# Optimization experiments

Measured on AMD Instinct MI355X. Metric: run time of the kernel, lower is better.

The kernel has to match this reference:

```python
import jax, jax.numpy as jnp
import numpy as np

SIGMA = 0.05
SIGMA2 = SIGMA * SIGMA
N_NODES = 100000
N_EDGES = 3200000


def setup_inputs() -> dict:
    key = jax.random.key(0)
    k1, k2, k3, k4 = jax.random.split(key, 4)
    source_points = jax.random.normal(k1, (N_NODES, 3), dtype=jnp.float32)
    target_points = jax.random.normal(k2, (N_NODES, 3), dtype=jnp.float32)
    edge_index = jax.random.randint(k3, (2, N_EDGES), 0, N_NODES, dtype=jnp.int64)
    edge_weights = jax.random.uniform(k4, (N_EDGES, 1), dtype=jnp.float32)
    return {"source_points": source_points, "target_points": target_points,
            "edge_index": edge_index, "edge_weights": edge_weights}


def reference(source_points, target_points, edge_index, edge_weights):
    N = source_points.shape[0]
    dst = edge_index[0]  # center point each edge contributes to
    nbr = edge_index[1]  # neighbor point index

    src_nb = source_points[nbr]            # [E,3]
    tgt_nb = target_points[nbr]            # [E,3]

    ones_e = jnp.ones((edge_index.shape[1],), dtype=source_points.dtype)
    counts = jnp.maximum(jax.ops.segment_sum(ones_e, dst, num_segments=N), 1.0)[:, None]
    src_centers = jax.ops.segment_sum(src_nb, dst, num_segments=N) / counts  # [N,3]
    tgt_centers = jax.ops.segment_sum(tgt_nb, dst, num_segments=N) / counts  # [N,3]

    src_diff = (src_nb - src_centers[dst]) * edge_weights  # [E,3]
    tgt_diff = tgt_nb - tgt_centers[dst]                   # [E,3]

    # per-edge outer product, scattered to per-point 3x3 covariances
    edge_mats = src_diff[:, :, None] * tgt_diff[:, None, :]          # [E,3,3]
    point_mats = jax.ops.segment_sum(edge_mats, dst, num_segments=N)  # [N,3,3]

    U, S, Vh = jnp.linalg.svd(point_mats)  # torch.svd's V = Vh^T, so U @ V^T == U @ Vh
    R0 = jnp.matmul(U, Vh)
    det = jnp.linalg.det(R0)
    ones_n = jnp.ones((N,), dtype=source_points.dtype)
    d_diag = jax.lax.stop_gradient(jnp.stack([ones_n, ones_n, det], axis=-1))  # [N,3]
    R = jnp.matmul(U * d_diag[:, None, :], Vh)  # U @ diag(d) @ Vh, proper rotation

    trans = tgt_centers - jnp.einsum('nij,nj->ni', R, src_centers)  # [N,3]

    # apply each neighbor's rigid transform and compute robust weights
    transformed = jnp.einsum('eij,ej->ei', R[nbr], src_nb) + trans[nbr]  # [E,3]
    d2 = jnp.sum(jnp.square(transformed - tgt_nb), axis=-1, keepdims=True)  # [E,1]
    new_edge_weights = SIGMA2 / (d2 + SIGMA2)
    return (R, trans, new_edge_weights)
```

## Files before the change

### kernel.cpp

```cpp
#include <hip/hip_runtime.h>
#include <math.h>

static constexpr float kSigma2 = 0.05f * 0.05f;
static constexpr int kCap2 = 2560;

__device__ __forceinline__ int load_idx(const void* ei, long long j, int is64) {
    if (is64) return (int)(((const long long*)ei)[j]);
    return ((const int*)ei)[j];
}

__global__ void k_detect(const int* __restrict__ ei32, int E, int* __restrict__ nz) {
    int t = threadIdx.x;
    int lim = E < 2048 ? E : 2048;
    int acc = 0;
    for (int k = t; k < lim; k += blockDim.x) acc |= ei32[2 * k + 1];
    if (acc) atomicOr(nz, 1);
}

__global__ void k_pack(const float* __restrict__ src, const float* __restrict__ tgt,
                       float4* __restrict__ s4, float4* __restrict__ t4, int N) {
    int i = blockIdx.x * blockDim.x + threadIdx.x;
    if (i >= N) return;
    s4[i] = make_float4(src[3 * i + 0], src[3 * i + 1], src[3 * i + 2], 0.0f);
    t4[i] = make_float4(tgt[3 * i + 0], tgt[3 * i + 1], tgt[3 * i + 2], 0.0f);
}

__device__ void kabsch_from_M(const double M[3][3], double Rm[3][3]) {
    Rm[0][0] = 1; Rm[0][1] = 0; Rm[0][2] = 0;
    Rm[1][0] = 0; Rm[1][1] = 1; Rm[1][2] = 0;
    Rm[2][0] = 0; Rm[2][1] = 0; Rm[2][2] = 1;

    double frob2 = 0.0;
#pragma unroll
    for (int r = 0; r < 3; ++r)
#pragma unroll
        for (int c = 0; c < 3; ++c) frob2 += M[r][c] * M[r][c];
    if (frob2 <= 1e-80) return;

    double A[3][3];
#pragma unroll
    for (int r = 0; r < 3; ++r)
#pragma unroll
        for (int c = 0; c < 3; ++c) {
            double s = 0.0;
#pragma unroll
            for (int k = 0; k < 3; ++k) s += M[k][r] * M[k][c];
            A[r][c] = s;
        }
    double V[3][3] = {{1, 0, 0}, {0, 1, 0}, {0, 0, 1}};
    const int PL[3] = {0, 0, 1};
    const int QL[3] = {1, 2, 2};
    for (int sweep = 0; sweep < 15; ++sweep) {
        double off = fabs(A[0][1]) + fabs(A[0][2]) + fabs(A[1][2]);
        if (off == 0.0) break;
        for (int pi = 0; pi < 3; ++pi) {
            int p = PL[pi], q = QL[pi], r3 = 3 - p - q;
            double apq = A[p][q];
            if (apq == 0.0) continue;
            double theta = (A[q][q] - A[p][p]) / (2.0 * apq);
            double t = copysign(1.0, theta) / (fabs(theta) + sqrt(theta * theta + 1.0));
            double c = 1.0 / sqrt(t * t + 1.0);
            double s = t * c;
            A[p][p] -= t * apq;
            A[q][q] += t * apq;
            A[p][q] = 0.0; A[q][p] = 0.0;
            double arp = A[r3][p], arq = A[r3][q];
            A[r3][p] = c * arp - s * arq; A[p][r3] = A[r3][p];
            A[r3][q] = s * arp + c * arq; A[q][r3] = A[r3][q];
#pragma unroll
            for (int k = 0; k < 3; ++k) {
                double vp = V[k][p], vq = V[k][q];
                V[k][p] = c * vp - s * vq;
                V[k][q] = s * vp + c * vq;
            }
        }
    }
    double lam[3] = {A[0][0], A[1][1], A[2][2]};
    int id0 = 0, id1 = 1, id2 = 2, tt;
    if (lam[id0] < lam[id1]) { tt = id0; id0 = id1; id1 = tt; }
    if (lam[id0] < lam[id2]) { tt = id0; id0 = id2; id2 = tt; }
    if (lam[id1] < lam[id2]) { tt = id1; id1 = id2; id2 = tt; }
    double v1[3] = {V[0][id0], V[1][id0], V[2][id0]};
    double v2[3] = {V[0][id1], V[1][id1], V[2][id1]};
    double v3[3] = {V[0][id2], V[1][id2], V[2][id2]};

    double b1[3], b2[3];
#pragma unroll
    for (int r = 0; r < 3; ++r) {
        b1[r] = M[r][0] * v1[0] + M[r][1] * v1[1] + M[r][2] * v1[2];
        b2[r] = M[r][0] * v2[0] + M[r][1] * v2[1] + M[r][2] * v2[2];
    }
    double n1 = sqrt(b1[0] * b1[0] + b1[1] * b1[1] + b1[2] * b1[2]);
    if (n1 <= 1e-150) return;
    double u1[3] = {b1[0] / n1, b1[1] / n1, b1[2] / n1};
    double dot = u1[0] * b2[0] + u1[1] * b2[1] + u1[2] * b2[2];
    double w2[3] = {b2[0] - dot * u1[0], b2[1] - dot * u1[1], b2[2] - dot * u1[2]};
    double n2 = sqrt(w2[0] * w2[0] + w2[1] * w2[1] + w2[2] * w2[2]);
    double u2[3];
    if (n2 > n1 * 1e-12) {
        u2[0] = w2[0] / n2; u2[1] = w2[1] / n2; u2[2] = w2[2] / n2;
    } else {
        double ex0 = (fabs(u1[0]) < 0.9) ? 1.0 : 0.0;
        double ex1 = 1.0 - ex0;
        double cx = u1[1] * 0.0 - u1[2] * ex1;
        double cy = u1[2] * ex0 - u1[0] * 0.0;
        double cz = u1[0] * ex1 - u1[1] * ex0;
        double cn = sqrt(cx * cx + cy * cy + cz * cz);
        u2[0] = cx / cn; u2[1] = cy / cn; u2[2] = cz / cn;
    }
    double u3[3] = {u1[1] * u2[2] - u1[2] * u2[1],
                    u1[2] * u2[0] - u1[0] * u2[2],
                    u1[0] * u2[1] - u1[1] * u2[0]};
    double dV = v1[0] * (v2[1] * v3[2] - v2[2] * v3[1])
              - v1[1] * (v2[0] * v3[2] - v2[2] * v3[0])
              + v1[2] * (v2[0] * v3[1] - v2[1] * v3[0]);
    dV = (dV >= 0.0) ? 1.0 : -1.0;
#pragma unroll
    for (int r = 0; r < 3; ++r)
#pragma unroll
        for (int c = 0; c < 3; ++c)
            Rm[r][c] = u1[r] * v1[c] + u2[r] * v2[c] + dV * u3[r] * v3[c];
}


__global__ void __launch_bounds__(256) k_bhist(const void* __restrict__ ei,
                                               int* __restrict__ thist,
                                               int* __restrict__ ccnt,
                                               const int* __restrict__ nz,
                                               int E, int N, int nbuckets,
                                               int ntiles16, int ntiles4) {
    __shared__ int lhist[2048];
    __shared__ int ccl[4][16];
    int t = threadIdx.x;
    int lane = t & 63;
    long long tile = (long long)blockIdx.x * 16384;
    long long remll = (long long)E - tile;
    int rem = (remll < 16384) ? (int)remll : 16384;
    int is64 = (*nz == 0);
    for (int i = t; i < 2048; i += 256) lhist[i] = 0;
    if (t < 64) ((int*)ccl)[t] = 0;
    __syncthreads();
    if (rem == 16384) {
        for (int it = 0; it < 8; ++it) {
            long long base = tile + (long long)it * 2048 + (long long)t * 8;
            int d[8];
            if (is64) {
                const long long* p = (const long long*)ei + base;
#pragma unroll
                for (int k = 0; k < 4; ++k) {
                    longlong2 v = ((const longlong2*)p)[k];
                    d[2 * k] = (int)v.x;
                    d[2 * k + 1] = (int)v.y;
                }
            } else {
                const int* p = (const int*)ei + base;
                int4 a = ((const int4*)p)[0];
                int4 bb = ((const int4*)p)[1];
                d[0] = a.x; d[1] = a.y; d[2] = a.z; d[3] = a.w;
                d[4] = bb.x; d[5] = bb.y; d[6] = bb.z; d[7] = bb.w;
            }
            int sub = it >> 1;
#pragma unroll
            for (int k = 0; k < 8; ++k) {
                int dk = d[k];
                int bin = ((unsigned)dk < (unsigned)N) ? (dk >> 13) : -1;
                if (bin >= 0) atomicAdd(&lhist[dk >> 6], 1);
                unsigned long long valid = __ballot(bin >= 0);
                unsigned long long v0 = __ballot(bin & 1);
                unsigned long long v1 = __ballot(bin & 2);
                unsigned long long v2 = __ballot(bin & 4);
                unsigned long long v3 = __ballot(bin & 8);
                if (lane < 16) {
                    unsigned long long m = valid;
                    m &= (lane & 1) ? v0 : ~v0;
                    m &= (lane & 2) ? v1 : ~v1;
                    m &= (lane & 4) ? v2 : ~v2;
                    m &= (lane & 8) ? v3 : ~v3;
                    int c = __popcll(m);
                    if (c > 0) atomicAdd(&ccl[sub][lane], c);
                }
            }
        }
    } else {
        for (int idx = t; idx < rem; idx += 256) {
            int dk = load_idx(ei, tile + idx, is64);
            if ((unsigned)dk < (unsigned)N) {
                atomicAdd(&lhist[dk >> 6], 1);
                atomicAdd(&ccl[idx >> 12][dk >> 13], 1);
            }
        }
    }
    __syncthreads();
    int* row = thist + (long long)blockIdx.x * 2048;
    for (int b = t; b < 2048; b += 256) row[b] = lhist[b];
    if (t < 64) {
        int sub = t >> 4, c = t & 15;
        long long st = (long long)blockIdx.x * 4 + sub;
        if (st < ntiles4) ccnt[st * 16 + c] = ccl[sub][c];
    }
}

__global__ void __launch_bounds__(256) k_bsum(const int* __restrict__ thist,
                                              int* __restrict__ btot, int ntiles16) {
    int t = threadIdx.x;
    int bin = blockIdx.x * 16 + (t >> 4);
    int j = t & 15;
    int s = 0;
    for (int i = j; i < ntiles16; i += 16) s += thist[(long long)i * 2048 + bin];
#pragma unroll
    for (int off = 8; off >= 1; off >>= 1) s += __shfl_down(s, off, 16);
    if (j == 0) btot[bin] = s;
}

__global__ void k_scan(const int* __restrict__ btot, int* __restrict__ boff,
                       int* __restrict__ cur16, int* __restrict__ curC16, int nbuckets) {
    __shared__ int sm[2048];
    int t = threadIdx.x;
    int v0 = (t < nbuckets) ? btot[t] : 0;
    int v1 = (t + 1024 < nbuckets) ? btot[t + 1024] : 0;
    sm[t] = v0;
    sm[t + 1024] = v1;
    __syncthreads();
    for (int s = 1; s < 2048; s <<= 1) {
        int x0 = (t >= s) ? sm[t - s] : 0;
        int x1 = (t + 1024 >= s) ? sm[t + 1024 - s] : 0;
        __syncthreads();
        sm[t] += x0;
        sm[t + 1024] += x1;
        __syncthreads();
    }
    if (t < nbuckets) {
        int ex = sm[t] - v0;
        boff[t] = ex;
        cur16[t * 16] = ex;
        if ((t & 127) == 0) curC16[(t >> 7) * 16] = ex;
    }
    int t2 = t + 1024;
    if (t2 < nbuckets) {
        int ex = sm[t2] - v1;
        boff[t2] = ex;
        cur16[t2 * 16] = ex;
        if ((t2 & 127) == 0) curC16[(t2 >> 7) * 16] = ex;
    }
    if (t == nbuckets - 1) boff[nbuckets] = sm[t];
    if (t2 == nbuckets - 1) boff[nbuckets] = sm[t2];
}

__global__ void __launch_bounds__(256) k_cscan(const int* __restrict__ ccnt,
                                               const int* __restrict__ boff,
                                               int* __restrict__ cbase,
                                               int ntiles, int nbuckets, int ncoarse) {
    __shared__ int sm[256];
    int c = blockIdx.x;
    int t = threadIdx.x;
    int f = c * 128;
    if (f > nbuckets) f = nbuckets;
    int run = boff[f];
    for (int start = 0; start < ntiles; start += 256) {
        int i = start + t;
        int v = (i < ntiles) ? ccnt[(long long)i * 16 + c] : 0;
        sm[t] = v;
        __syncthreads();
        for (int s = 1; s < 256; s <<= 1) {
            int x = (t >= s) ? sm[t - s] : 0;
            __syncthreads();
            sm[t] += x;
            __syncthreads();
        }
        if (i < ntiles) cbase[(long long)i * 16 + c] = run + sm[t] - v;
        int tot = sm[255];
        __syncthreads();
        run += tot;
    }
}

__global__ void __launch_bounds__(256) k_cscatter(const void* __restrict__ ei,
                                                  const float* __restrict__ ew,
                                                  const int* __restrict__ cbase,
                                                  int2* __restrict__ sedge1,
                                                  const int* __restrict__ nz,
                                                  int E, int N, int ncoarse) {
    __shared__ int2 stage[4096];
    __shared__ unsigned char binOf[4096];
    __shared__ int hist[16];
    __shared__ int excl[16];
    __shared__ int gbase[16];
    __shared__ int woffs[4][16];
    __shared__ int wbase[4][16];
    int t = threadIdx.x;
    int w = t >> 6, lane = t & 63;
    unsigned long long lanebelow = ((unsigned long long)1 << lane) - 1;
    long long tile = (long long)blockIdx.x * 4096;
    long long remll = (long long)E - tile;
    int rem = (remll < 4096) ? (int)remll : 4096;
    int is64 = (*nz == 0);
    if (t < 16) hist[t] = 0;
    if (t < 64) ((int*)woffs)[t] = 0;
    __syncthreads();

    int mybin[16];
    int mypos[16];
    int2 mypay[16];
#pragma unroll
    for (int h = 0; h < 2; ++h) {
        int dd[8], nn[8];
        float ww[8];
        int cnt8 = 0;
        int coff = h * 2048 + t * 8;
        long long cb = tile + coff;
        if (coff + 8 <= rem) {
            if (is64) {
                const long long* pd = (const long long*)ei + cb;
                const long long* pn = (const long long*)ei + (long long)E + cb;
#pragma unroll
                for (int k = 0; k < 4; ++k) {
                    longlong2 vd = ((const longlong2*)pd)[k];
                    longlong2 vn = ((const longlong2*)pn)[k];
                    dd[2 * k] = (int)vd.x; dd[2 * k + 1] = (int)vd.y;
                    nn[2 * k] = (int)vn.x; nn[2 * k + 1] = (int)vn.y;
                }
            } else {
                const int* pd = (const int*)ei + cb;
                const int* pn = (const int*)ei + (long long)E + cb;
                int4 a = ((const int4*)pd)[0], b = ((const int4*)pd)[1];
                int4 c = ((const int4*)pn)[0], d = ((const int4*)pn)[1];
                dd[0] = a.x; dd[1] = a.y; dd[2] = a.z; dd[3] = a.w;
                dd[4] = b.x; dd[5] = b.y; dd[6] = b.z; dd[7] = b.w;
                nn[0] = c.x; nn[1] = c.y; nn[2] = c.z; nn[3] = c.w;
                nn[4] = d.x; nn[5] = d.y; nn[6] = d.z; nn[7] = d.w;
            }
            const float* pw = ew + cb;
            float4 wa = ((const float4*)pw)[0], wb = ((const float4*)pw)[1];
            ww[0] = wa.x; ww[1] = wa.y; ww[2] = wa.z; ww[3] = wa.w;
            ww[4] = wb.x; ww[5] = wb.y; ww[6] = wb.z; ww[7] = wb.w;
            cnt8 = 8;
        } else {
#pragma unroll
            for (int k = 0; k < 8; ++k) {
                if (coff + k < rem) {
                    dd[cnt8] = load_idx(ei, cb + k, is64);
                    nn[cnt8] = load_idx(ei, (long long)E + cb + k, is64);
                    ww[cnt8] = ew[cb + k];
                    ++cnt8;
                }
            }
        }
#pragma unroll
        for (int k = 0; k < 8; ++k) {
            int r = h * 8 + k;
            int bin = -1;
            if (k < cnt8) {
                int d = dd[k];
                if ((unsigned)d < (unsigned)N) {
                    int n = nn[k];
                    if ((unsigned)n >= (unsigned)N) n = N;
                    bin = d >> 13;
                    mypay[r].x = (n << 13) | (d & 8191);
                    mypay[r].y = __float_as_int(ww[k]);
                }
            }
            mybin[r] = bin;
            unsigned long long valid = __ballot(bin >= 0);
            unsigned long long v0 = __ballot(bin & 1);
            unsigned long long v1 = __ballot(bin & 2);
            unsigned long long v2 = __ballot(bin & 4);
            unsigned long long v3 = __ballot(bin & 8);
            if (bin >= 0) {
                unsigned long long m = valid;
                m &= (bin & 1) ? v0 : ~v0;
                m &= (bin & 2) ? v1 : ~v1;
                m &= (bin & 4) ? v2 : ~v2;
                m &= (bin & 8) ? v3 : ~v3;
                int rank = __popcll(m & lanebelow);
                int cnt = __popcll(m);
                int cur = woffs[w][bin];
                mypos[r] = cur + rank;
                if (rank == 0) woffs[w][bin] = cur + cnt;
            }
        }
    }
    __syncthreads();
    if (t < 64) {
        int w2 = t >> 4, b = t & 15;
        int c = woffs[w2][b];
        wbase[w2][b] = (c > 0) ? atomicAdd(&hist[b], c) : 0;
    }
    __syncthreads();
    if (t == 0) {
        int run = 0;
#pragma unroll
        for (int c = 0; c < 16; ++c) { excl[c] = run; run += hist[c]; }
    }
    __syncthreads();
#pragma unroll
    for (int r = 0; r < 16; ++r) {
        if (mybin[r] >= 0) {
            int lpos = excl[mybin[r]] + wbase[w][mybin[r]] + mypos[r];
            stage[lpos] = mypay[r];
            binOf[lpos] = (unsigned char)mybin[r];
        }
    }
    if (t < 16) gbase[t] = cbase[(long long)blockIdx.x * 16 + t];
    __syncthreads();
    int total = excl[15] + hist[15];
    for (int lpos = t; lpos < total; lpos += 256) {
        int c = binOf[lpos];
        sedge1[(long long)gbase[c] + (lpos - excl[c])] = stage[lpos];
    }
}

__global__ void __launch_bounds__(256) k_fscatter(const int2* __restrict__ sedge1,
                                                  int* __restrict__ cur16,
                                                  const int* __restrict__ boff,
                                                  int2* __restrict__ sedge2,
                                                  int E, int nbuckets, int ncoarse) {
    __shared__ int2 stage[2048];
    __shared__ unsigned short binOf[2048];
    __shared__ int lhist[1024];
    __shared__ int lincl[1024];
    __shared__ int gbase[1024];
    __shared__ int co[17];
    __shared__ int s_clo, s_W;
    int t = threadIdx.x;
    if (t <= ncoarse) {
        int f = t * 128;
        if (f > nbuckets) f = nbuckets;
        co[t] = boff[f];
    }
    __syncthreads();
    int Ev = co[ncoarse];
    long long tile = (long long)blockIdx.x * 2048;
    if (tile >= Ev) return;
    long long remll = (long long)Ev - tile;
    int rem = (remll < 2048) ? (int)remll : 2048;

    if (t == 0) {
        long long p0 = tile, p1 = tile + rem - 1;
        int c0 = 0;
        while (c0 + 1 < ncoarse && p0 >= co[c0 + 1]) ++c0;
        int c1 = c0;
        while (c1 + 1 < ncoarse && p1 >= co[c1 + 1]) ++c1;
        s_clo = c0;
        s_W = (c1 - c0 + 1) * 128;
    }
    __syncthreads();
    int clo = s_clo, W = s_W;

    int2 pay[8];
    int cnt8 = 0;
    if (rem == 2048) {
        const int4* p4 = (const int4*)(sedge1 + tile + (long long)t * 8);
#pragma unroll
        for (int k = 0; k < 4; ++k) {
            int4 v = p4[k];
            pay[2 * k].x = v.x; pay[2 * k].y = v.y;
            pay[2 * k + 1].x = v.z; pay[2 * k + 1].y = v.w;
        }
        cnt8 = 8;
    } else {
        int base = t * 8;
#pragma unroll
        for (int k = 0; k < 8; ++k) {
            int idx = base + k;
            if (idx < rem) pay[cnt8++] = sedge1[tile + idx];
        }
    }

    if (W > 1024) {
        for (int k = 0; k < cnt8; ++k) {
            long long pos = tile + t * 8 + k;
            int c = clo;
            while (c + 1 < ncoarse && pos >= co[c + 1]) ++c;
            int x1 = pay[k].x;
            unsigned nbr = ((unsigned)x1) >> 13;
            int fin = c * 128 + ((x1 & 8191) >> 6);
            int gpos = atomicAdd(&cur16[fin * 16], 1);
            int2 out;
            out.x = (int)((nbr << 6) | (unsigned)(x1 & 63));
            out.y = pay[k].y;
            sedge2[gpos] = out;
        }
        return;
    }

    for (int i = t; i < W; i += 256) lhist[i] = 0;
    __syncthreads();

    int mybin[8], myrank[8];
    int2 mypay[8];
#pragma unroll
    for (int k = 0; k < 8; ++k) {
        mybin[k] = -1;
        if (k < cnt8) {
            long long pos = tile + t * 8 + k;
            int c = clo;
            while (c + 1 < ncoarse && pos >= co[c + 1]) ++c;
            int x1 = pay[k].x;
            unsigned nbr = ((unsigned)x1) >> 13;
            int rel = (c - clo) * 128 + ((x1 & 8191) >> 6);
            mybin[k] = rel;
            myrank[k] = atomicAdd(&lhist[rel], 1);
            mypay[k].x = (int)((nbr << 6) | (unsigned)(x1 & 63));
            mypay[k].y = pay[k].y;
        }
    }
    __syncthreads();
    for (int i = t; i < W; i += 256) lincl[i] = lhist[i];
    __syncthreads();
    for (int s = 1; s < W; s <<= 1) {
        int tmp[4];
        int cj = 0;
        for (int i = t; i < W; i += 256) tmp[cj++] = (i >= s) ? lincl[i - s] : 0;
        __syncthreads();
        cj = 0;
        for (int i = t; i < W; i += 256) lincl[i] += tmp[cj++];
        __syncthreads();
    }
#pragma unroll
    for (int k = 0; k < 8; ++k) {
        if (mybin[k] >= 0) {
            int ex = lincl[mybin[k]] - lhist[mybin[k]];
            int lpos = ex + myrank[k];
            stage[lpos] = mypay[k];
            binOf[lpos] = (unsigned short)mybin[k];
        }
    }
    __syncthreads();
    for (int rel = t; rel < W; rel += 256) {
        int c = lhist[rel];
        int fin = clo * 128 + rel;
        gbase[rel] = (c > 0 && fin < nbuckets) ? atomicAdd(&cur16[fin * 16], c) : 0;
    }
    __syncthreads();
    int total = lincl[W - 1];
    for (int lpos = t; lpos < total; lpos += 256) {
        int rel = binOf[lpos];
        int ex = lincl[rel] - lhist[rel];
        sedge2[gbase[rel] + (lpos - ex)] = stage[lpos];
    }
}

__global__ void __launch_bounds__(256) k_binscatter(const void* __restrict__ ei,
                                                    const float* __restrict__ ew,
                                                    int* __restrict__ cur16,
                                                    int2* __restrict__ sedge,
                                                    const int* __restrict__ nz,
                                                    int E, int N, int nbuckets) {
    __shared__ int2 stage[2048];
    __shared__ unsigned short binOf[2048];
    __shared__ int lhist[2048];
    __shared__ int lincl[2048];
    __shared__ int gbase[2048];
    int t = threadIdx.x;
    long long tile = (long long)blockIdx.x * 2048;
    long long remll = (long long)E - tile;
    int rem = (remll < 2048) ? (int)remll : 2048;
    int is64 = (*nz == 0);
    for (int i = t; i < 2048; i += 256) lhist[i] = 0;
    __syncthreads();

    int dd[8], nn[8];
    float ww[8];
    int cnt8 = 0;
    if (rem == 2048) {
        if (is64) {
            const long long* pd = (const long long*)ei + tile + (long long)t * 8;
            const long long* pn = (const long long*)ei + (long long)E + tile + (long long)t * 8;
#pragma unroll
            for (int k = 0; k < 4; ++k) {
                longlong2 vd = ((const longlong2*)pd)[k];
                longlong2 vn = ((const longlong2*)pn)[k];
                dd[2 * k] = (int)vd.x; dd[2 * k + 1] = (int)vd.y;
                nn[2 * k] = (int)vn.x; nn[2 * k + 1] = (int)vn.y;
            }
        } else {
            const int* pd = (const int*)ei + tile + (long long)t * 8;
            const int* pn = (const int*)ei + (long long)E + tile + (long long)t * 8;
            int4 a = ((const int4*)pd)[0], b = ((const int4*)pd)[1];
            int4 c = ((const int4*)pn)[0], d = ((const int4*)pn)[1];
            dd[0] = a.x; dd[1] = a.y; dd[2] = a.z; dd[3] = a.w;
            dd[4] = b.x; dd[5] = b.y; dd[6] = b.z; dd[7] = b.w;
            nn[0] = c.x; nn[1] = c.y; nn[2] = c.z; nn[3] = c.w;
            nn[4] = d.x; nn[5] = d.y; nn[6] = d.z; nn[7] = d.w;
        }
        const float* pw = ew + tile + (long long)t * 8;
        float4 wa = ((const float4*)pw)[0], wb = ((const float4*)pw)[1];
        ww[0] = wa.x; ww[1] = wa.y; ww[2] = wa.z; ww[3] = wa.w;
        ww[4] = wb.x; ww[5] = wb.y; ww[6] = wb.z; ww[7] = wb.w;
        cnt8 = 8;
    } else {
        int base = t * 8;
#pragma unroll
        for (int k = 0; k < 8; ++k) {
            int idx = base + k;
            if (idx < rem) {
                long long e = tile + idx;
                dd[cnt8] = load_idx(ei, e, is64);
                nn[cnt8] = load_idx(ei, (long long)E + e, is64);
                ww[cnt8] = ew[e];
                ++cnt8;
            }
        }
    }

    int mybin[8];
    int myrank[8];
    int2 mypay[8];
#pragma unroll
    for (int k = 0; k < 8; ++k) {
        mybin[k] = -1;
        if (k < cnt8) {
            int d = dd[k];
            if ((unsigned)d < (unsigned)N) {
                int n = nn[k];
                if ((unsigned)n >= (unsigned)N) n = N;
                int bb = d >> 6;
                mybin[k] = bb;
                myrank[k] = atomicAdd(&lhist[bb], 1);
                mypay[k].x = (n << 6) | (d & 63);
                mypay[k].y = __float_as_int(ww[k]);
            }
        }
    }
    __syncthreads();
    for (int i = t; i < 2048; i += 256) lincl[i] = lhist[i];
    __syncthreads();
    for (int s = 1; s < 2048; s <<= 1) {
        int tmp[8];
#pragma unroll
        for (int j = 0; j < 8; ++j) {
            int i = (j << 8) + t;
            tmp[j] = (i >= s) ? lincl[i - s] : 0;
        }
        __syncthreads();
#pragma unroll
        for (int j = 0; j < 8; ++j) {
            int i = (j << 8) + t;
            lincl[i] += tmp[j];
        }
        __syncthreads();
    }
#pragma unroll
    for (int k = 0; k < 8; ++k) {
        if (mybin[k] >= 0) {
            int ex = lincl[mybin[k]] - lhist[mybin[k]];
            int lpos = ex + myrank[k];
            stage[lpos] = mypay[k];
            binOf[lpos] = (unsigned short)mybin[k];
        }
    }
    __syncthreads();
    for (int bb = t; bb < 2048; bb += 256) {
        int c = lhist[bb];
        gbase[bb] = (c > 0 && bb < nbuckets) ? atomicAdd(&cur16[bb * 16], c) : 0;
    }
    __syncthreads();
    int total = lincl[2047];
    for (int lpos = t; lpos < total; lpos += 256) {
        int bb = binOf[lpos];
        int ex = lincl[bb] - lhist[bb];
        sedge[gbase[bb] + (lpos - ex)] = stage[lpos];
    }
}

__global__ void __launch_bounds__(256) k_sortmoment(const int* __restrict__ boff,
                                                    const int2* __restrict__ sedge2,
                                                    const float4* __restrict__ s4,
                                                    const float4* __restrict__ t4,
                                                    float* __restrict__ momG, int N) {
    __shared__ int2 sorted[kCap2];
    __shared__ int hist[64];
    __shared__ int offs[64];
    __shared__ int scanbuf[64];
    __shared__ int woffs[4][64];
    __shared__ int wbase[4][64];
    int b = blockIdx.x, t = threadIdx.x;
    int w = t >> 6, lane = t & 63;
    unsigned long long lanebelow = ((unsigned long long)1 << lane) - 1;
    int e0 = boff[b], e1 = boff[b + 1];
    int cnt = e1 - e0;
    int inlds = (cnt <= kCap2);
    if (t < 64) hist[t] = 0;
    ((int*)woffs)[t] = 0;
    __syncthreads();
    if (inlds) {
        int2 pay[10];
        int mypos[10];
#pragma unroll
        for (int r = 0; r < 10; ++r) {
            int idx = r * 256 + t;
            int bin = -1;
            if (idx < cnt) {
                pay[r] = sedge2[e0 + idx];
                bin = pay[r].x & 63;
            }
            unsigned long long vm = __ballot(bin >= 0);
            unsigned long long b0 = __ballot(bin & 1);
            unsigned long long b1 = __ballot(bin & 2);
            unsigned long long b2 = __ballot(bin & 4);
            unsigned long long b3 = __ballot(bin & 8);
            unsigned long long b4 = __ballot(bin & 16);
            unsigned long long b5 = __ballot(bin & 32);
            if (bin >= 0) {
                unsigned long long m = vm;
                m &= (bin & 1) ? b0 : ~b0;
                m &= (bin & 2) ? b1 : ~b1;
                m &= (bin & 4) ? b2 : ~b2;
                m &= (bin & 8) ? b3 : ~b3;
                m &= (bin & 16) ? b4 : ~b4;
                m &= (bin & 32) ? b5 : ~b5;
                int rank = __popcll(m & lanebelow);
                int cm = __popcll(m);
                int curv = woffs[w][bin];
                mypos[r] = curv + rank;
                if (rank == 0) woffs[w][bin] = curv + cm;
            }
        }
        __syncthreads();
        {
            int w2 = t >> 6, bb = t & 63;
            int c = woffs[w2][bb];
            wbase[w2][bb] = (c > 0) ? atomicAdd(&hist[bb], c) : 0;
        }
        __syncthreads();
        if (t < 64) scanbuf[t] = hist[t];
        __syncthreads();
        for (int s = 1; s < 64; s <<= 1) {
            int v = 0;
            if (t < 64 && t >= s) v = scanbuf[t - s];
            __syncthreads();
            if (t < 64) scanbuf[t] += v;
            __syncthreads();
        }
        if (t < 64) offs[t] = scanbuf[t] - hist[t];
        __syncthreads();
#pragma unroll
        for (int r = 0; r < 10; ++r) {
            int idx = r * 256 + t;
            if (idx < cnt) {
                int bin = pay[r].x & 63;
                sorted[offs[bin] + wbase[w][bin] + mypos[r]] = pay[r];
            }
        }
        __syncthreads();
    }
    int oct = t >> 3, lane8 = t & 7;
#pragma unroll
    for (int rr = 0; rr < 2; ++rr) {
        int nl = oct + rr * 32;
        long long node = (long long)b * 64 + nl;
        float v[23];
#pragma unroll
        for (int i = 0; i < 23; ++i) v[i] = 0.0f;
        if (node < N) {
            if (inlds) {
                int start = offs[nl];
                int cn = hist[nl];
                for (int j = lane8; j < cn; j += 8) {
                    int2 p = sorted[start + j];
                    unsigned n = ((unsigned)p.x) >> 6;
                    if (n >= (unsigned)N) continue;
                    float w_ = __int_as_float(p.y);
                    float4 a = s4[n];
                    float4 bb = t4[n];
                    float sx = a.x, sy = a.y, sz = a.z;
                    float tx = bb.x, ty = bb.y, tz = bb.z;
                    v[0] += 1.0f;
                    v[1] += sx; v[2] += sy; v[3] += sz;
                    v[4] += tx; v[5] += ty; v[6] += tz;
                    v[7] += w_;
                    float wsx = w_ * sx, wsy = w_ * sy, wsz = w_ * sz;
                    v[8] += wsx; v[9] += wsy; v[10] += wsz;
                    v[11] += w_ * tx; v[12] += w_ * ty; v[13] += w_ * tz;
                    v[14] += wsx * tx; v[15] += wsx * ty; v[16] += wsx * tz;
                    v[17] += wsy * tx; v[18] += wsy * ty; v[19] += wsy * tz;
                    v[20] += wsz * tx; v[21] += wsz * ty; v[22] += wsz * tz;
                }
            } else {
                for (int j = lane8; j < cnt; j += 8) {
                    int2 p = sedge2[e0 + j];
                    if ((p.x & 63) != nl) continue;
                    unsigned n = ((unsigned)p.x) >> 6;
                    if (n >= (unsigned)N) continue;
                    float w_ = __int_as_float(p.y);
                    float4 a = s4[n];
                    float4 bb = t4[n];
                    float sx = a.x, sy = a.y, sz = a.z;
                    float tx = bb.x, ty = bb.y, tz = bb.z;
                    v[0] += 1.0f;
                    v[1] += sx; v[2] += sy; v[3] += sz;
                    v[4] += tx; v[5] += ty; v[6] += tz;
                    v[7] += w_;
                    float wsx = w_ * sx, wsy = w_ * sy, wsz = w_ * sz;
                    v[8] += wsx; v[9] += wsy; v[10] += wsz;
                    v[11] += w_ * tx; v[12] += w_ * ty; v[13] += w_ * tz;
                    v[14] += wsx * tx; v[15] += wsx * ty; v[16] += wsx * tz;
                    v[17] += wsy * tx; v[18] += wsy * ty; v[19] += wsy * tz;
                    v[20] += wsz * tx; v[21] += wsz * ty; v[22] += wsz * tz;
                }
            }
        }
#pragma unroll
        for (int m = 1; m < 8; m <<= 1) {
#pragma unroll
            for (int i = 0; i < 23; ++i) v[i] += __shfl_xor(v[i], m, 64);
        }
        if (lane8 == 0 && node < N) {
#pragma unroll
            for (int i = 0; i < 23; ++i) momG[(size_t)i * N + node] = v[i];
        }
    }
}

__global__ void __launch_bounds__(256) k_kabsch2(const float* __restrict__ momG,
                                                 const float4* __restrict__ s4,
                                                 const float4* __restrict__ t4,
                                                 float* __restrict__ Rout,
                                                 float* __restrict__ Tout,
                                                 float* __restrict__ wnode, int N) {
    int i = blockIdx.x * blockDim.x + threadIdx.x;
    if (i >= N) return;
    float m[23];
#pragma unroll
    for (int k = 0; k < 23; ++k) m[k] = momG[(size_t)k * N + i];
    double cntv = (double)m[0];
    double inv = 1.0 / fmax(cntv, 1.0);
    double sb[3] = {m[1] * inv, m[2] * inv, m[3] * inv};
    double tb[3] = {m[4] * inv, m[5] * inv, m[6] * inv};
    double Sw = m[7];
    double Sws[3] = {m[8], m[9], m[10]};
    double Swt[3] = {m[11], m[12], m[13]};
    double M[3][3];
#pragma unroll
    for (int r = 0; r < 3; ++r)
#pragma unroll
        for (int c = 0; c < 3; ++c)
            M[r][c] = (double)m[14 + 3 * r + c]
                    - sb[r] * Swt[c] - Sws[r] * tb[c] + Sw * sb[r] * tb[c];
    double Rm[3][3];
    kabsch_from_M(M, Rm);
    double T0 = tb[0] - (Rm[0][0] * sb[0] + Rm[0][1] * sb[1] + Rm[0][2] * sb[2]);
    double T1 = tb[1] - (Rm[1][0] * sb[0] + Rm[1][1] * sb[1] + Rm[1][2] * sb[2]);
    double T2 = tb[2] - (Rm[2][0] * sb[0] + Rm[2][1] * sb[1] + Rm[2][2] * sb[2]);
#pragma unroll
    for (int r = 0; r < 3; ++r)
#pragma unroll
        for (int c = 0; c < 3; ++c)
            Rout[9 * (long long)i + 3 * r + c] = (float)Rm[r][c];
    Tout[3 * i + 0] = (float)T0;
    Tout[3 * i + 1] = (float)T1;
    Tout[3 * i + 2] = (float)T2;
    float4 a = s4[i];
    float4 q = t4[i];
    double x0 = Rm[0][0] * a.x + Rm[0][1] * a.y + Rm[0][2] * a.z + T0;
    double x1 = Rm[1][0] * a.x + Rm[1][1] * a.y + Rm[1][2] * a.z + T1;
    double x2 = Rm[2][0] * a.x + Rm[2][1] * a.y + Rm[2][2] * a.z + T2;
    double d0 = x0 - q.x, d1 = x1 - q.y, d2 = x2 - q.z;
    double dd = d0 * d0 + d1 * d1 + d2 * d2;
    wnode[i] = (float)((double)kSigma2 / (dd + (double)kSigma2));
}

__global__ void __launch_bounds__(256) k_wgather(const void* __restrict__ ei,
                                                 const float* __restrict__ wnode,
                                                 float* __restrict__ wout,
                                                 const int* __restrict__ nz,
                                                 int E, int N) {
    int gid = blockIdx.x * blockDim.x + threadIdx.x;
    long long base = (long long)gid * 8;
    if (base >= E) return;
    int is64 = (*nz == 0);
    int n_[8];
    int full = (base + 8 <= (long long)E);
    if (full) {
        if (is64) {
            const long long* p = (const long long*)ei + (long long)E + base;
#pragma unroll
            for (int k = 0; k < 4; ++k) {
                longlong2 a = ((const longlong2*)p)[k];
                n_[2 * k] = (int)a.x;
                n_[2 * k + 1] = (int)a.y;
            }
        } else {
            const int* p = (const int*)ei + (long long)E + base;
            int4 a = ((const int4*)p)[0];
            int4 b = ((const int4*)p)[1];
            n_[0] = a.x; n_[1] = a.y; n_[2] = a.z; n_[3] = a.w;
            n_[4] = b.x; n_[5] = b.y; n_[6] = b.z; n_[7] = b.w;
        }
        float w[8];
#pragma unroll
        for (int k = 0; k < 8; ++k)
            w[k] = ((unsigned)n_[k] < (unsigned)N) ? wnode[n_[k]] : 1.0f;
        *(float4*)(wout + base) = make_float4(w[0], w[1], w[2], w[3]);
        *(float4*)(wout + base + 4) = make_float4(w[4], w[5], w[6], w[7]);
    } else {
#pragma unroll
        for (int k = 0; k < 8; ++k) {
            long long e = base + k;
            if (e < E) {
                int n = load_idx(ei, (long long)E + e, is64);
                wout[e] = ((unsigned)n < (unsigned)N) ? wnode[n] : 1.0f;
            }
        }
    }
}


__global__ void k_accum1(const void* __restrict__ ei, const float* __restrict__ src,
                         const float* __restrict__ tgt, float* __restrict__ cnt,
                         float* __restrict__ ssum, float* __restrict__ tsum,
                         const int* __restrict__ nz, int E, int N) {
    int e = blockIdx.x * blockDim.x + threadIdx.x;
    if (e >= E) return;
    int is64 = (*nz == 0);
    int d = load_idx(ei, e, is64);
    int n = load_idx(ei, (long long)E + e, is64);
    if ((unsigned)d >= (unsigned)N || (unsigned)n >= (unsigned)N) return;
    atomicAdd(&cnt[d], 1.0f);
    atomicAdd(&ssum[3 * d + 0], src[3 * n + 0]);
    atomicAdd(&ssum[3 * d + 1], src[3 * n + 1]);
    atomicAdd(&ssum[3 * d + 2], src[3 * n + 2]);
    atomicAdd(&tsum[3 * d + 0], tgt[3 * n + 0]);
    atomicAdd(&tsum[3 * d + 1], tgt[3 * n + 1]);
    atomicAdd(&tsum[3 * d + 2], tgt[3 * n + 2]);
}

__global__ void k_centers(float* __restrict__ cnt, float* __restrict__ ssum,
                          float* __restrict__ tsum, int N) {
    int i = blockIdx.x * blockDim.x + threadIdx.x;
    if (i >= N) return;
    float inv = 1.0f / fmaxf(cnt[i], 1.0f);
    ssum[3 * i + 0] *= inv; ssum[3 * i + 1] *= inv; ssum[3 * i + 2] *= inv;
    tsum[3 * i + 0] *= inv; tsum[3 * i + 1] *= inv; tsum[3 * i + 2] *= inv;
}

__global__ void k_accum2(const void* __restrict__ ei, const float* __restrict__ src,
                         const float* __restrict__ tgt, const float* __restrict__ ew,
                         const float* __restrict__ sc, const float* __restrict__ tc,
                         float* __restrict__ Mm, const int* __restrict__ nz, int E, int N) {
    int e = blockIdx.x * blockDim.x + threadIdx.x;
    if (e >= E) return;
    int is64 = (*nz == 0);
    int d = load_idx(ei, e, is64);
    int n = load_idx(ei, (long long)E + e, is64);
    if ((unsigned)d >= (unsigned)N || (unsigned)n >= (unsigned)N) return;
    float w = ew[e];
    float a0 = (src[3 * n + 0] - sc[3 * d + 0]) * w;
    float a1 = (src[3 * n + 1] - sc[3 * d + 1]) * w;
    float a2 = (src[3 * n + 2] - sc[3 * d + 2]) * w;
    float b0 = tgt[3 * n + 0] - tc[3 * d + 0];
    float b1 = tgt[3 * n + 1] - tc[3 * d + 1];
    float b2 = tgt[3 * n + 2] - tc[3 * d + 2];
    float* Md = Mm + 9 * (long long)d;
    atomicAdd(Md + 0, a0 * b0); atomicAdd(Md + 1, a0 * b1); atomicAdd(Md + 2, a0 * b2);
    atomicAdd(Md + 3, a1 * b0); atomicAdd(Md + 4, a1 * b1); atomicAdd(Md + 5, a1 * b2);
    atomicAdd(Md + 6, a2 * b0); atomicAdd(Md + 7, a2 * b1); atomicAdd(Md + 8, a2 * b2);
}

__global__ void k_kabsch(const float* __restrict__ Mm, const float* __restrict__ sc,
                         const float* __restrict__ tc, float* __restrict__ Rout,
                         float* __restrict__ Tout, int N) {
    int i = blockIdx.x * blockDim.x + threadIdx.x;
    if (i >= N) return;
    double M[3][3];
#pragma unroll
    for (int r = 0; r < 3; ++r)
#pragma unroll
        for (int c = 0; c < 3; ++c)
            M[r][c] = (double)Mm[9 * (long long)i + 3 * r + c];
    double Rm[3][3];
    kabsch_from_M(M, Rm);
    double s0 = sc[3 * i + 0], s1 = sc[3 * i + 1], s2 = sc[3 * i + 2];
    double t0 = tc[3 * i + 0], t1 = tc[3 * i + 1], t2 = tc[3 * i + 2];
#pragma unroll
    for (int r = 0; r < 3; ++r)
#pragma unroll
        for (int c = 0; c < 3; ++c)
            Rout[9 * (long long)i + 3 * r + c] = (float)Rm[r][c];
    Tout[3 * i + 0] = (float)(t0 - (Rm[0][0] * s0 + Rm[0][1] * s1 + Rm[0][2] * s2));
    Tout[3 * i + 1] = (float)(t1 - (Rm[1][0] * s0 + Rm[1][1] * s1 + Rm[1][2] * s2));
    Tout[3 * i + 2] = (float)(t2 - (Rm[2][0] * s0 + Rm[2][1] * s1 + Rm[2][2] * s2));
}

__global__ void k_weights_plain(const void* __restrict__ ei,
                                const float* __restrict__ src,
                                const float* __restrict__ tgt,
                                const float* __restrict__ R,
                                const float* __restrict__ T,
                                float* __restrict__ wout,
                                const int* __restrict__ nz, int E, int N) {
    int e = blockIdx.x * blockDim.x + threadIdx.x;
    if (e >= E) return;
    int is64 = (*nz == 0);
    int n = load_idx(ei, (long long)E + e, is64);
    float w = 1.0f;
    if ((unsigned)n < (unsigned)N) {
        float p0 = src[3 * n + 0], p1 = src[3 * n + 1], p2 = src[3 * n + 2];
        float q0 = tgt[3 * n + 0], q1 = tgt[3 * n + 1], q2 = tgt[3 * n + 2];
        const float* Rn = R + 9 * (long long)n;
        const float* Tn = T + 3 * (long long)n;
        float x0 = Rn[0] * p0 + Rn[1] * p1 + Rn[2] * p2 + Tn[0];
        float x1 = Rn[3] * p0 + Rn[4] * p1 + Rn[5] * p2 + Tn[1];
        float x2 = Rn[6] * p0 + Rn[7] * p1 + Rn[8] * p2 + Tn[2];
        float d0 = x0 - q0, d1 = x1 - q1, d2 = x2 - q2;
        float dd = d0 * d0 + d1 * d1 + d2 * d2;
        w = kSigma2 / (dd + kSigma2);
    }
    wout[e] = w;
}

extern "C" void kernel_launch(void* const* d_in, const int* in_sizes, int n_in,
                              void* d_out, int out_size, void* d_ws, size_t ws_size,
                              hipStream_t stream) {
    const float* src = (const float*)d_in[0];
    const float* tgt = (const float*)d_in[1];
    const void* ei = d_in[2];
    const float* ew = (const float*)d_in[3];
    int N = in_sizes[0] / 3;
    int E = in_sizes[3];

    float* out = (float*)d_out;
    float* Rout = out;
    float* Tout = out + (size_t)9 * N;
    float* Wout = out + (size_t)12 * N;

    int eb = (E + 255) / 256;
    int nb = (N + 255) / 256;
    int nbuckets = (N + 63) / 64;
    int ncoarse = (nbuckets + 127) / 128;
    int tiles = (int)(((long long)E + 2047) / 2048);
    int ntiles4 = (int)(((long long)E + 4095) / 4096);
    int ntiles16 = (int)(((long long)E + 16383) / 16384);
    int wb8 = (int)(((long long)E + 2047) / 2048);

    size_t ctrl_ints = 16 + 2048 + (size_t)nbuckets * 16 + 256
                     + (size_t)(nbuckets + 1) + (size_t)ntiles4 * 16 * 2
                     + (size_t)ntiles16 * 2048;
    ctrl_ints = (ctrl_ints + 3) & ~(size_t)3;
    size_t after1 = ctrl_ints + 2 * (size_t)E;
    after1 = (after1 + 3) & ~(size_t)3;
    size_t after2 = after1 + 2 * (size_t)E;
    after2 = (after2 + 3) & ~(size_t)3;
    size_t tail_ints = 8 * (size_t)N + (size_t)N + 23 * (size_t)N;
    size_t needA = (after2 + tail_ints) * sizeof(int);
    size_t needB = (after1 + tail_ints) * sizeof(int);

    if (N <= 131072 && nbuckets <= 2048 && ws_size >= needB) {
        int twolevel = (ws_size >= needA) ? 1 : 0;
        int* nz = (int*)d_ws;
        int* btot = nz + 16;
        int* cur16 = btot + 2048;
        int* curC16 = cur16 + (size_t)nbuckets * 16;
        int* boff = curC16 + 256;
        int* ccnt = boff + (nbuckets + 1);
        int* cbase = ccnt + (size_t)ntiles4 * 16;
        int* thist = cbase + (size_t)ntiles4 * 16;
        int2* sedge1 = (int2*)((int*)d_ws + ctrl_ints);
        size_t tail_base = twolevel ? after2 : after1;
        int2* sedge2 = twolevel ? (int2*)((int*)d_ws + after1) : sedge1;
        float4* s4 = (float4*)((int*)d_ws + tail_base);
        float4* t4 = s4 + N;
        float* wnode = (float*)(t4 + N);
        float* momG = wnode + N;

        hipMemsetAsync(d_ws, 0, 16 * sizeof(int), stream);

        k_detect<<<1, 256, 0, stream>>>((const int*)ei, E, nz);
        k_pack<<<nb, 256, 0, stream>>>(src, tgt, s4, t4, N);
        k_bhist<<<ntiles16, 256, 0, stream>>>(ei, thist, ccnt, nz, E, N, nbuckets,
                                              ntiles16, ntiles4);
        k_bsum<<<128, 256, 0, stream>>>(thist, btot, ntiles16);
        k_scan<<<1, 1024, 0, stream>>>(btot, boff, cur16, curC16, nbuckets);
        if (twolevel) {
            k_cscan<<<16, 256, 0, stream>>>(ccnt, boff, cbase, ntiles4, nbuckets, ncoarse);
            k_cscatter<<<ntiles4, 256, 0, stream>>>(ei, ew, cbase, sedge1, nz, E, N, ncoarse);
            k_fscatter<<<tiles, 256, 0, stream>>>(sedge1, cur16, boff, sedge2, E, nbuckets, ncoarse);
        } else {
            k_binscatter<<<tiles, 256, 0, stream>>>(ei, ew, cur16, sedge2, nz, E, N, nbuckets);
        }
        k_sortmoment<<<nbuckets, 256, 0, stream>>>(boff, sedge2, s4, t4, momG, N);
        k_kabsch2<<<nb, 256, 0, stream>>>(momG, s4, t4, Rout, Tout, wnode, N);
        k_wgather<<<wb8, 256, 0, stream>>>(ei, wnode, Wout, nz, E, N);
    } else {
        float* cnt = (float*)d_ws;
        float* ssum = cnt + N;
        float* tsum = ssum + 3 * (size_t)N;
        float* Mm = tsum + 3 * (size_t)N;
        int* nz = (int*)(Mm + 9 * (size_t)N);
        size_t ws_bytes = (size_t)16 * N * sizeof(float) + 16;
        hipMemsetAsync(d_ws, 0, ws_bytes, stream);
        k_detect<<<1, 256, 0, stream>>>((const int*)ei, E, nz);
        k_accum1<<<eb, 256, 0, stream>>>(ei, src, tgt, cnt, ssum, tsum, nz, E, N);
        k_centers<<<nb, 256, 0, stream>>>(cnt, ssum, tsum, N);
        k_accum2<<<eb, 256, 0, stream>>>(ei, src, tgt, ew, ssum, tsum, Mm, nz, E, N);
        k_kabsch<<<nb, 256, 0, stream>>>(Mm, ssum, tsum, Rout, Tout, N);
        k_weights_plain<<<eb, 256, 0, stream>>>(ei, src, tgt, Rout, Tout, Wout, nz, E, N);
    }
}
```

Baseline: 242.8 us.

## Interleave source/target points and unroll moment gather loop by two

Packs source and target points into one interleaved float4 array, so each neighbor gather reads 32 contiguous bytes (one cache line region) instead of two separate lines. The LDS-path moment loop is unrolled to issue two edges' gathers before accumulating, which raises memory-level parallelism; loads are hoisted above the bounds check, with the workspace padded to allow this. The Jacobi SVD now stops on a relative off-diagonal threshold rather than exact zero, cutting sweeps at some accuracy risk.

```diff
diff --git a/kernel.cpp b/kernel.cpp
--- a/kernel.cpp
+++ b/kernel.cpp
@@ -18,11 +18,11 @@
 }
 
 __global__ void k_pack(const float* __restrict__ src, const float* __restrict__ tgt,
-                       float4* __restrict__ s4, float4* __restrict__ t4, int N) {
+                       float4* __restrict__ pt, int N) {
     int i = blockIdx.x * blockDim.x + threadIdx.x;
     if (i >= N) return;
-    s4[i] = make_float4(src[3 * i + 0], src[3 * i + 1], src[3 * i + 2], 0.0f);
-    t4[i] = make_float4(tgt[3 * i + 0], tgt[3 * i + 1], tgt[3 * i + 2], 0.0f);
+    pt[2 * i] = make_float4(src[3 * i + 0], src[3 * i + 1], src[3 * i + 2], 0.0f);
+    pt[2 * i + 1] = make_float4(tgt[3 * i + 0], tgt[3 * i + 1], tgt[3 * i + 2], 0.0f);
 }
 
 __device__ void kabsch_from_M(const double M[3][3], double Rm[3][3]) {
@@ -50,9 +50,10 @@
     double V[3][3] = {{1, 0, 0}, {0, 1, 0}, {0, 0, 1}};
     const int PL[3] = {0, 0, 1};
     const int QL[3] = {1, 2, 2};
+    double thr = 1e-14 * frob2;
     for (int sweep = 0; sweep < 15; ++sweep) {
         double off = fabs(A[0][1]) + fabs(A[0][2]) + fabs(A[1][2]);
-        if (off == 0.0) break;
+        if (off <= thr) break;
         for (int pi = 0; pi < 3; ++pi) {
             int p = PL[pi], q = QL[pi], r3 = 3 - p - q;
             double apq = A[p][q];
@@ -663,10 +664,24 @@
     }
 }
 
+__device__ __forceinline__ void mom_acc(float v[23], float w_, float4 a, float4 bb) {
+    float sx = a.x, sy = a.y, sz = a.z;
+    float tx = bb.x, ty = bb.y, tz = bb.z;
+    v[0] += 1.0f;
+    v[1] += sx; v[2] += sy; v[3] += sz;
+    v[4] += tx; v[5] += ty; v[6] += tz;
+    v[7] += w_;
+    float wsx = w_ * sx, wsy = w_ * sy, wsz = w_ * sz;
+    v[8] += wsx; v[9] += wsy; v[10] += wsz;
+    v[11] += w_ * tx; v[12] += w_ * ty; v[13] += w_ * tz;
+    v[14] += wsx * tx; v[15] += wsx * ty; v[16] += wsx * tz;
+    v[17] += wsy * tx; v[18] += wsy * ty; v[19] += wsy * tz;
+    v[20] += wsz * tx; v[21] += wsz * ty; v[22] += wsz * tz;
+}
+
 __global__ void __launch_bounds__(256) k_sortmoment(const int* __restrict__ boff,
                                                     const int2* __restrict__ sedge2,
-                                                    const float4* __restrict__ s4,
-                                                    const float4* __restrict__ t4,
+                                                    const float4* __restrict__ pt,
                                                     float* __restrict__ momG, int N) {
     __shared__ int2 sorted[kCap2];
     __shared__ int hist[64];
@@ -756,25 +771,22 @@
             if (inlds) {
                 int start = offs[nl];
                 int cn = hist[nl];
-                for (int j = lane8; j < cn; j += 8) {
+                int j = lane8;
+                for (; j + 8 < cn; j += 16) {
+                    int2 p1 = sorted[start + j];
+                    int2 p2 = sorted[start + j + 8];
+                    unsigned n1 = ((unsigned)p1.x) >> 6;
+                    unsigned n2 = ((unsigned)p2.x) >> 6;
+                    float4 a1 = pt[2 * n1], b1v = pt[2 * n1 + 1];
+                    float4 a2 = pt[2 * n2], b2v = pt[2 * n2 + 1];
+                    if (n1 < (unsigned)N) mom_acc(v, __int_as_float(p1.y), a1, b1v);
+                    if (n2 < (unsigned)N) mom_acc(v, __int_as_float(p2.y), a2, b2v);
+                }
+                if (j < cn) {
                     int2 p = sorted[start + j];
                     unsigned n = ((unsigned)p.x) >> 6;
-                    if (n >= (unsigned)N) continue;
-                    float w_ = __int_as_float(p.y);
-                    float4 a = s4[n];
-                    float4 bb = t4[n];
-                    float sx = a.x, sy = a.y, sz = a.z;
-                    float tx = bb.x, ty = bb.y, tz = bb.z;
-                    v[0] += 1.0f;
-                    v[1] += sx; v[2] += sy; v[3] += sz;
-                    v[4] += tx; v[5] += ty; v[6] += tz;
-                    v[7] += w_;
-                    float wsx = w_ * sx, wsy = w_ * sy, wsz = w_ * sz;
-                    v[8] += wsx; v[9] += wsy; v[10] += wsz;
-                    v[11] += w_ * tx; v[12] += w_ * ty; v[13] += w_ * tz;
-                    v[14] += wsx * tx; v[15] += wsx * ty; v[16] += wsx * tz;
-                    v[17] += wsy * tx; v[18] += wsy * ty; v[19] += wsy * tz;
-                    v[20] += wsz * tx; v[21] += wsz * ty; v[22] += wsz * tz;
+                    float4 a = pt[2 * n], bb = pt[2 * n + 1];
+                    if (n < (unsigned)N) mom_acc(v, __int_as_float(p.y), a, bb);
                 }
             } else {
                 for (int j = lane8; j < cnt; j += 8) {
@@ -782,21 +794,8 @@
                     if ((p.x & 63) != nl) continue;
                     unsigned n = ((unsigned)p.x) >> 6;
                     if (n >= (unsigned)N) continue;
-                    float w_ = __int_as_float(p.y);
-                    float4 a = s4[n];
-                    float4 bb = t4[n];
-                    float sx = a.x, sy = a.y, sz = a.z;
-                    float tx = bb.x, ty = bb.y, tz = bb.z;
-                    v[0] += 1.0f;
-                    v[1] += sx; v[2] += sy; v[3] += sz;
-                    v[4] += tx; v[5] += ty; v[6] += tz;
-                    v[7] += w_;
-                    float wsx = w_ * sx, wsy = w_ * sy, wsz = w_ * sz;
-                    v[8] += wsx; v[9] += wsy; v[10] += wsz;
-                    v[11] += w_ * tx; v[12] += w_ * ty; v[13] += w_ * tz;
-                    v[14] += wsx * tx; v[15] += wsx * ty; v[16] += wsx * tz;
-                    v[17] += wsy * tx; v[18] += wsy * ty; v[19] += wsy * tz;
-                    v[20] += wsz * tx; v[21] += wsz * ty; v[22] += wsz * tz;
+                    float4 a = pt[2 * n], bb = pt[2 * n + 1];
+                    mom_acc(v, __int_as_float(p.y), a, bb);
                 }
             }
         }
@@ -813,8 +812,7 @@
 }
 
 __global__ void __launch_bounds__(256) k_kabsch2(const float* __restrict__ momG,
-                                                 const float4* __restrict__ s4,
-                                                 const float4* __restrict__ t4,
+                                                 const float4* __restrict__ pt,
                                                  float* __restrict__ Rout,
                                                  float* __restrict__ Tout,
                                                  float* __restrict__ wnode, int N) {
@@ -850,8 +848,8 @@
     Tout[3 * i + 0] = (float)T0;
     Tout[3 * i + 1] = (float)T1;
     Tout[3 * i + 2] = (float)T2;
-    float4 a = s4[i];
-    float4 q = t4[i];
+    float4 a = pt[2 * i];
+    float4 q = pt[2 * i + 1];
     double x0 = Rm[0][0] * a.x + Rm[0][1] * a.y + Rm[0][2] * a.z + T0;
     double x1 = Rm[1][0] * a.x + Rm[1][1] * a.y + Rm[1][2] * a.z + T1;
     double x2 = Rm[2][0] * a.x + Rm[2][1] * a.y + Rm[2][2] * a.z + T2;
@@ -1041,7 +1039,7 @@
     after1 = (after1 + 3) & ~(size_t)3;
     size_t after2 = after1 + 2 * (size_t)E;
     after2 = (after2 + 3) & ~(size_t)3;
-    size_t tail_ints = 8 * (size_t)N + (size_t)N + 23 * (size_t)N;
+    size_t tail_ints = 8 * (size_t)(N + 1) + (size_t)N + 23 * (size_t)N;
     size_t needA = (after2 + tail_ints) * sizeof(int);
     size_t needB = (after1 + tail_ints) * sizeof(int);
 
@@ -1058,15 +1056,14 @@
         int2* sedge1 = (int2*)((int*)d_ws + ctrl_ints);
         size_t tail_base = twolevel ? after2 : after1;
         int2* sedge2 = twolevel ? (int2*)((int*)d_ws + after1) : sedge1;
-        float4* s4 = (float4*)((int*)d_ws + tail_base);
-        float4* t4 = s4 + N;
-        float* wnode = (float*)(t4 + N);
+        float4* pt = (float4*)((int*)d_ws + tail_base);
+        float* wnode = (float*)(pt + 2 * (size_t)(N + 1));
         float* momG = wnode + N;
 
         hipMemsetAsync(d_ws, 0, 16 * sizeof(int), stream);
 
         k_detect<<<1, 256, 0, stream>>>((const int*)ei, E, nz);
-        k_pack<<<nb, 256, 0, stream>>>(src, tgt, s4, t4, N);
+        k_pack<<<nb, 256, 0, stream>>>(src, tgt, pt, N);
         k_bhist<<<ntiles16, 256, 0, stream>>>(ei, thist, ccnt, nz, E, N, nbuckets,
                                               ntiles16, ntiles4);
         k_bsum<<<128, 256, 0, stream>>>(thist, btot, ntiles16);
@@ -1078,8 +1075,8 @@
         } else {
             k_binscatter<<<tiles, 256, 0, stream>>>(ei, ew, cur16, sedge2, nz, E, N, nbuckets);
         }
-        k_sortmoment<<<nbuckets, 256, 0, stream>>>(boff, sedge2, s4, t4, momG, N);
-        k_kabsch2<<<nb, 256, 0, stream>>>(momG, s4, t4, Rout, Tout, wnode, N);
+        k_sortmoment<<<nbuckets, 256, 0, stream>>>(boff, sedge2, pt, momG, N);
+        k_kabsch2<<<nb, 256, 0, stream>>>(momG, pt, Rout, Tout, wnode, N);
         k_wgather<<<wb8, 256, 0, stream>>>(ei, wnode, Wout, nz, E, N);
     } else {
         float* cnt = (float*)d_ws;
```

Measured after the change: 232.1 us. -4.4%, faster.
